# Kernel optimization log

Hardware: AMD Instinct MI355X
Metric: run time of the kernel (lower is better)

## Reference

```python
import jax, jax.numpy as jnp
import numpy as np

B, S, D_IN = 2, 2048, 2048
H, G, HD = 16, 4, 128          # num_heads, num_kv_groups, head_dim
GROUP = H // G                  # 4 query heads per kv group
D_OUT = H * HD                  # 2048
EPS = 1e-6


def _rope_tables(seq_len, head_dim, theta=10000.0):
    inv = 1.0 / (theta ** (np.arange(0, head_dim, 2, dtype=np.float32) / head_dim))
    pos = np.arange(seq_len, dtype=np.float32)
    ang = np.outer(pos, inv)                      # [S, HD/2]
    ang = np.concatenate([ang, ang], axis=-1)     # [S, HD]
    return jnp.asarray(np.cos(ang)), jnp.asarray(np.sin(ang))


def setup_inputs() -> dict:
    key = jax.random.key(0)
    ks = jax.random.split(key, 6)
    x = jax.random.normal(ks[0], (B, S, D_IN), dtype=jnp.float32)
    # Linear weights stored as [in, out] so y = x @ W (same math as nn.Linear)
    Wq = jax.random.normal(ks[1], (D_IN, 2 * D_OUT), dtype=jnp.float32) * (D_IN ** -0.5)
    Wk = jax.random.normal(ks[2], (D_IN, G * HD), dtype=jnp.float32) * (D_IN ** -0.5)
    Wv = jax.random.normal(ks[3], (D_IN, G * HD), dtype=jnp.float32) * (D_IN ** -0.5)
    Wo = jax.random.normal(ks[4], (D_OUT, D_IN), dtype=jnp.float32) * (D_OUT ** -0.5)
    q_norm_w = jnp.zeros((HD,), dtype=jnp.float32)  # Qwen-style zero-init (scale = 1 + w)
    k_norm_w = jnp.zeros((HD,), dtype=jnp.float32)
    cos, sin = _rope_tables(S, HD)
    mask = jnp.triu(jnp.ones((S, S), dtype=bool), k=1)  # causal: True above diagonal is masked
    return {"x": x, "Wq": Wq, "Wk": Wk, "Wv": Wv, "Wo": Wo,
            "q_norm_w": q_norm_w, "k_norm_w": k_norm_w,
            "cos": cos, "sin": sin, "mask": mask}


def _rmsnorm(x, w):
    xf = x.astype(jnp.float32)
    n = xf * jax.lax.rsqrt(jnp.mean(xf * xf, axis=-1, keepdims=True) + EPS)
    return (n * (1.0 + w.astype(jnp.float32))).astype(x.dtype)


def _apply_rope(x, cos, sin):
    # x: [..., S, HD]; full-dim rotation (rot_dim == head_dim)
    s = x.shape[-2]
    c = cos[:s][None, None]
    sn = sin[:s][None, None]
    x1, x2 = x[..., : HD // 2], x[..., HD // 2 :]
    rotated = jnp.concatenate([-x2, x1], axis=-1)
    return (x * c + rotated * sn).astype(x.dtype)


def reference(x, Wq, Wk, Wv, Wo, q_norm_w, k_norm_w, cos, sin, mask):
    b, s, _ = x.shape
    qg = (x @ Wq).reshape(b, s, H, 2 * HD)
    q, gate = qg[..., :HD], qg[..., HD:]
    gate = gate.reshape(b, s, D_OUT)
    q = q.transpose(0, 2, 1, 3)                                 # [b,H,s,HD]
    k = (x @ Wk).reshape(b, s, G, HD).transpose(0, 2, 1, 3)     # [b,G,s,HD]
    v = (x @ Wv).reshape(b, s, G, HD).transpose(0, 2, 1, 3)
    q = _rmsnorm(q, q_norm_w)
    k = _rmsnorm(k, k_norm_w)
    q = _apply_rope(q, cos, sin)
    k = _apply_rope(k, cos, sin)
    # GQA: group query heads by kv group instead of repeat_interleave on k/v
    qg4 = q.reshape(b, G, GROUP, s, HD)
    scores = jnp.einsum("bgjqd,bgkd->bgjqk", qg4, k)            # [b,G,GROUP,s,s]
    scores = jnp.where(mask[None, None, None], -jnp.inf, scores)
    w = jax.nn.softmax((scores * (HD ** -0.5)).astype(jnp.float32), axis=-1).astype(q.dtype)
    ctx = jnp.einsum("bgjqk,bgkd->bgjqd", w, v)                 # [b,G,GROUP,s,HD]
    ctx = ctx.reshape(b, H, s, HD).transpose(0, 2, 1, 3).reshape(b, s, D_OUT)
    ctx = ctx * jax.nn.sigmoid(gate)
    return ctx @ Wo
```

## Files before the change

### kernel.cpp

```cpp
#include <hip/hip_runtime.h>

#define S_LEN 2048
#define NROWS 4096
#define DIN   2048
#define DQKV  5120
#define DQG   4096

typedef __bf16 bf16x8 __attribute__((ext_vector_type(8)));
typedef float  floatx4 __attribute__((ext_vector_type(4)));
typedef unsigned short u16;

#define QK_SCALE 0.08838834764831845f

__device__ __forceinline__ u16 f2bf(float f) {
  unsigned int u = __float_as_uint(f);
  u += 0x7fffu + ((u >> 16) & 1u);
  return (u16)(u >> 16);
}
__device__ __forceinline__ float bf2f(u16 v) {
  return __uint_as_float(((unsigned int)v) << 16);
}
__device__ __forceinline__ int swz(int col, int row) {
  return (col & ~63) | ((((col >> 3) & 7) ^ (row & 7)) << 3) | (col & 7);
}

__device__ __forceinline__ void gload_lds16(const void* g, void* l) {
  __builtin_amdgcn_global_load_lds(
      (__attribute__((address_space(1))) void*)(void*)(g),
      (__attribute__((address_space(3))) void*)(l), 16, 0, 0);
}

__device__ __forceinline__ void tcvt_body(const float* __restrict__ src,
                                          u16* __restrict__ dst,
                                          int C, int dld, int bx, int by,
                                          float (*tile)[33]) {
  const int c0 = bx * 32, r0 = by * 32;
  const int t = threadIdx.x;
  {
    const int rl = t >> 3, cl4 = (t & 7) * 4;
    const float4 v = *reinterpret_cast<const float4*>(src + (size_t)(r0 + rl) * C + c0 + cl4);
    tile[rl][cl4 + 0] = v.x; tile[rl][cl4 + 1] = v.y;
    tile[rl][cl4 + 2] = v.z; tile[rl][cl4 + 3] = v.w;
  }
  __syncthreads();
  {
    const int cl = t >> 3, rl4 = (t & 7) * 4;
    ushort4 o;
    o.x = f2bf(tile[rl4 + 0][cl]); o.y = f2bf(tile[rl4 + 1][cl]);
    o.z = f2bf(tile[rl4 + 2][cl]); o.w = f2bf(tile[rl4 + 3][cl]);
    const int rd = c0 + cl, cd = r0 + rl4;
    *reinterpret_cast<ushort4*>(dst + (size_t)rd * dld + swz(cd, rd)) = o;
  }
}

__global__ __launch_bounds__(256) void prep(const float* __restrict__ x,
                                            const float* __restrict__ Wq,
                                            const float* __restrict__ Wk,
                                            const float* __restrict__ Wv,
                                            const float* __restrict__ Wo,
                                            u16* __restrict__ xb,
                                            u16* __restrict__ WqkvT,
                                            u16* __restrict__ WoT) {
  __shared__ float tile[32][33];
  const int bid = blockIdx.x;
  if (bid < 8192) {
    const int i = bid * 256 + threadIdx.x;
    const int row = i >> 9, col = (i & 511) << 2;
    const float4 v = reinterpret_cast<const float4*>(x)[i];
    ushort4 o;
    o.x = f2bf(v.x); o.y = f2bf(v.y); o.z = f2bf(v.z); o.w = f2bf(v.w);
    *reinterpret_cast<ushort4*>(xb + (size_t)row * DIN + swz(col, row)) = o;
  } else if (bid < 16384) {
    const int l = bid - 8192;
    tcvt_body(Wq, WqkvT, 4096, 2048, l & 127, l >> 7, tile);
  } else if (bid < 17408) {
    const int l = bid - 16384;
    tcvt_body(Wk, WqkvT + (size_t)4096 * 2048, 512, 2048, l & 15, l >> 4, tile);
  } else if (bid < 18432) {
    const int l = bid - 17408;
    tcvt_body(Wv, WqkvT + (size_t)4608 * 2048, 512, 2048, l & 15, l >> 4, tile);
  } else {
    const int l = bid - 18432;
    tcvt_body(Wo, WoT, 2048, 2048, l & 63, l >> 6, tile);
  }
}

template <bool BF16_OUT>
__global__ __launch_bounds__(256) void gemm_bt(const u16* __restrict__ A,
                                               const u16* __restrict__ Bt,
                                               void* __restrict__ Cv,
                                               int M, int N, int K, int ldc) {
  __shared__ __align__(16) u16 As[128 * 64];
  __shared__ __align__(16) u16 Bs[128 * 64];
  const int tid = threadIdx.x, wv = tid >> 6, lane = tid & 63;
  const int m0 = blockIdx.y * 128, n0 = blockIdx.x * 128;
  const int wm = (wv >> 1) * 64, wn = (wv & 1) * 64;
  const int frow = lane & 15, quad = lane >> 4, fsw = frow & 7;
  const int srow = lane >> 3, scol = (lane & 7) * 8;
  floatx4 acc[4][4] = {};
  for (int k0 = 0; k0 < K; k0 += 64) {
#pragma unroll
    for (int i = 0; i < 4; ++i) {
      const int rr = (wv * 4 + i) * 8;
      gload_lds16(A  + (size_t)(m0 + rr + srow) * K + k0 + scol, &As[rr * 64]);
      gload_lds16(Bt + (size_t)(n0 + rr + srow) * K + k0 + scol, &Bs[rr * 64]);
    }
    __syncthreads();
#pragma unroll
    for (int ks = 0; ks < 2; ++ks) {
      bf16x8 af[4], bfr[4];
#pragma unroll
      for (int mi = 0; mi < 4; ++mi)
        af[mi] = *reinterpret_cast<const bf16x8*>(
            &As[(wm + mi * 16 + frow) * 64 + (((ks * 4 + quad) ^ fsw) << 3)]);
#pragma unroll
      for (int ni = 0; ni < 4; ++ni)
        bfr[ni] = *reinterpret_cast<const bf16x8*>(
            &Bs[(wn + ni * 16 + frow) * 64 + (((ks * 4 + quad) ^ fsw) << 3)]);
#pragma unroll
      for (int mi = 0; mi < 4; ++mi)
#pragma unroll
        for (int ni = 0; ni < 4; ++ni)
          acc[mi][ni] = __builtin_amdgcn_mfma_f32_16x16x32_bf16(af[mi], bfr[ni], acc[mi][ni], 0, 0, 0);
    }
    __syncthreads();
  }
  const int crow = (lane >> 4) * 4, ccol = lane & 15;
#pragma unroll
  for (int mi = 0; mi < 4; ++mi)
#pragma unroll
    for (int ni = 0; ni < 4; ++ni) {
      const size_t base = (size_t)(m0 + wm + mi * 16 + crow) * ldc + (n0 + wn + ni * 16 + ccol);
      if constexpr (BF16_OUT) {
        u16* C = (u16*)Cv;
#pragma unroll
        for (int r = 0; r < 4; ++r) C[base + (size_t)r * ldc] = f2bf(acc[mi][ni][r]);
      } else {
        float* C = (float*)Cv;
#pragma unroll
        for (int r = 0; r < 4; ++r) C[base + (size_t)r * ldc] = acc[mi][ni][r];
      }
    }
}

__global__ __launch_bounds__(512, 2) void gemm256(const u16* __restrict__ A,
                                                  const u16* __restrict__ Bt,
                                                  u16* __restrict__ C,
                                                  int K, int ldc) {
  __shared__ __align__(16) u16 As[2][256 * 64];
  __shared__ __align__(16) u16 Bs[2][256 * 64];
  const int tid = threadIdx.x, wv = tid >> 6, lane = tid & 63;
  const int nx = gridDim.x;
  const int orig = blockIdx.y * nx + blockIdx.x;
  const int cpx = (nx * gridDim.y) >> 3;
  const int wgid = (orig & 7) * cpx + (orig >> 3);
  const int m0 = (wgid / nx) * 256, n0 = (wgid % nx) * 256;
  const int wm = (wv >> 2) * 128, wn = (wv & 3) * 64;
  const int f = lane & 15, quad = lane >> 4, fs = f & 7;

  const u16* Ab = A  + (size_t)(m0 + wv * 8 + (lane >> 3)) * K + (lane & 7) * 8;
  const u16* Bb = Bt + (size_t)(n0 + wv * 8 + (lane >> 3)) * K + (lane & 7) * 8;

  floatx4 acc[8][4] = {};
  bf16x8 af[4], bfr[4];

  auto stageA = [&](int sl, int t, int u) {
    gload_lds16(Ab + (size_t)u * 64 * K + (size_t)t * 64, &As[sl][(u * 64 + wv * 8) * 64]);
  };
  auto stageB = [&](int sl, int t, int u) {
    gload_lds16(Bb + (size_t)u * 64 * K + (size_t)t * 64, &Bs[sl][(u * 64 + wv * 8) * 64]);
  };
  auto loadA = [&](int sl, int fh, int ks) {
#pragma unroll
    for (int mf = 0; mf < 4; ++mf)
      af[mf] = *reinterpret_cast<const bf16x8*>(
          &As[sl][(wm + fh * 64 + mf * 16 + f) * 64 + ((((ks << 2) + quad) ^ fs) << 3)]);
  };
  auto loadB = [&](int sl, int ks) {
#pragma unroll
    for (int nf = 0; nf < 4; ++nf)
      bfr[nf] = *reinterpret_cast<const bf16x8*>(
          &Bs[sl][(wn + nf * 16 + f) * 64 + ((((ks << 2) + quad) ^ fs) << 3)]);
  };
  auto mmas = [&](int fh) {
#pragma unroll
    for (int mf = 0; mf < 4; ++mf)
#pragma unroll
      for (int nf = 0; nf < 4; ++nf)
        acc[fh * 4 + mf][nf] = __builtin_amdgcn_mfma_f32_16x16x32_bf16(
            af[mf], bfr[nf], acc[fh * 4 + mf][nf], 0, 0, 0);
  };

#pragma unroll
  for (int u = 0; u < 4; ++u) stageA(0, 0, u);
#pragma unroll
  for (int u = 0; u < 4; ++u) stageB(0, 0, u);
  stageA(1, 1, 0); stageA(1, 1, 2); stageB(1, 1, 0);
  asm volatile("s_waitcnt vmcnt(3)" ::: "memory");
  __builtin_amdgcn_s_barrier();

  const int IT = K >> 7;
#pragma unroll 1
  for (int i = 0; i < IT; ++i) {
    const int t0 = 2 * i;
    const bool st = (i < IT - 1);
    loadA(0, 0, 0); loadB(0, 0);
    stageA(1, t0 + 1, 1); stageA(1, t0 + 1, 3); stageB(1, t0 + 1, 1);
    __builtin_amdgcn_s_barrier();
    asm volatile("s_waitcnt lgkmcnt(0)" ::: "memory");
    __builtin_amdgcn_s_setprio(1); mmas(0); __builtin_amdgcn_s_setprio(0);
    __builtin_amdgcn_s_barrier();
    loadA(0, 1, 0);
    stageB(1, t0 + 1, 2); stageB(1, t0 + 1, 3);
    __builtin_amdgcn_s_barrier();
    asm volatile("s_waitcnt lgkmcnt(0)" ::: "memory");
    __builtin_amdgcn_s_setprio(1); mmas(1); __builtin_amdgcn_s_setprio(0);
    __builtin_amdgcn_s_barrier();
    loadA(0, 0, 1); loadB(0, 1);
    __builtin_amdgcn_s_barrier();
    asm volatile("s_waitcnt lgkmcnt(0)" ::: "memory");
    __builtin_amdgcn_s_setprio(1); mmas(0); __builtin_amdgcn_s_setprio(0);
    __builtin_amdgcn_s_barrier();
    loadA(0, 1, 1);
    if (st) { stageA(0, t0 + 2, 0); stageA(0, t0 + 2, 2); stageB(0, t0 + 2, 0); }
    __builtin_amdgcn_s_barrier();
    asm volatile("s_waitcnt lgkmcnt(0)" ::: "memory");
    __builtin_amdgcn_s_setprio(1); mmas(1); __builtin_amdgcn_s_setprio(0);
    if (st) { asm volatile("s_waitcnt vmcnt(3)" ::: "memory"); }
    else    { asm volatile("s_waitcnt vmcnt(0)" ::: "memory"); }
    __builtin_amdgcn_s_barrier();
    loadA(1, 0, 0); loadB(1, 0);
    if (st) { stageA(0, t0 + 2, 1); stageA(0, t0 + 2, 3); stageB(0, t0 + 2, 1); }
    __builtin_amdgcn_s_barrier();
    asm volatile("s_waitcnt lgkmcnt(0)" ::: "memory");
    __builtin_amdgcn_s_setprio(1); mmas(0); __builtin_amdgcn_s_setprio(0);
    __builtin_amdgcn_s_barrier();
    loadA(1, 1, 0);
    if (st) { stageB(0, t0 + 2, 2); stageB(0, t0 + 2, 3); }
    __builtin_amdgcn_s_barrier();
    asm volatile("s_waitcnt lgkmcnt(0)" ::: "memory");
    __builtin_amdgcn_s_setprio(1); mmas(1); __builtin_amdgcn_s_setprio(0);
    __builtin_amdgcn_s_barrier();
    loadA(1, 0, 1); loadB(1, 1);
    __builtin_amdgcn_s_barrier();
    asm volatile("s_waitcnt lgkmcnt(0)" ::: "memory");
    __builtin_amdgcn_s_setprio(1); mmas(0); __builtin_amdgcn_s_setprio(0);
    __builtin_amdgcn_s_barrier();
    loadA(1, 1, 1);
    if (st) { stageA(1, t0 + 3, 0); stageA(1, t0 + 3, 2); stageB(1, t0 + 3, 0); }
    __builtin_amdgcn_s_barrier();
    asm volatile("s_waitcnt lgkmcnt(0)" ::: "memory");
    __builtin_amdgcn_s_setprio(1); mmas(1); __builtin_amdgcn_s_setprio(0);
    if (st) { asm volatile("s_waitcnt vmcnt(3)" ::: "memory"); }
    __builtin_amdgcn_s_barrier();
  }

#pragma unroll
  for (int mf = 0; mf < 8; ++mf)
#pragma unroll
    for (int nf = 0; nf < 4; ++nf) {
      const size_t base = (size_t)(m0 + wm + (mf >> 2) * 64 + (mf & 3) * 16 + quad * 4) * ldc
                        + (n0 + wn + nf * 16 + f);
#pragma unroll
      for (int r = 0; r < 4; ++r) C[base + (size_t)r * ldc] = f2bf(acc[mf][nf][r]);
    }
}

__global__ __launch_bounds__(256) void postproj(const u16* __restrict__ QKV,
                                                const float* __restrict__ qw,
                                                const float* __restrict__ kw,
                                                const float* __restrict__ cosT,
                                                const float* __restrict__ sinT,
                                                u16* __restrict__ Qb,
                                                u16* __restrict__ Kb,
                                                u16* __restrict__ Vt) {
  __shared__ u16 tile[32][40];
  const int bid = blockIdx.x;
  const int wv = threadIdx.x >> 6, lane = threadIdx.x & 63;
  if (bid < 16384) {
    const int idx = bid * 4 + wv;
    const int h = idx & 15, row = idx >> 4;
    const int s = row & (S_LEN - 1), b = row >> 11;
    const u16* base = QKV + (size_t)row * DQKV + h * 256;
    const float v0 = bf2f(base[lane]), v1 = bf2f(base[lane + 64]);
    float ss = v0 * v0 + v1 * v1;
#pragma unroll
    for (int m = 32; m >= 1; m >>= 1) ss += __shfl_xor(ss, m);
    const float rn = rsqrtf(ss * (1.0f / 128.0f) + 1e-6f) * QK_SCALE;
    const float n0 = v0 * rn * (1.0f + qw[lane]);
    const float n1 = v1 * rn * (1.0f + qw[lane + 64]);
    const float c0 = cosT[(size_t)s * 128 + lane], c1 = cosT[(size_t)s * 128 + lane + 64];
    const float sn0 = sinT[(size_t)s * 128 + lane], sn1 = sinT[(size_t)s * 128 + lane + 64];
    u16* qb = Qb + ((size_t)(b * 16 + h) * S_LEN + s) * 128;
    qb[lane]      = f2bf(n0 * c0 - n1 * sn0);
    qb[lane + 64] = f2bf(n1 * c1 + n0 * sn1);
  } else if (bid < 20480) {
    const int idx = (bid - 16384) * 4 + wv;
    const int g = idx & 3, row = idx >> 2;
    const int s = row & (S_LEN - 1), b = row >> 11;
    const u16* base = QKV + (size_t)row * DQKV + DQG + g * 128;
    const float v0 = bf2f(base[lane]), v1 = bf2f(base[lane + 64]);
    float ss = v0 * v0 + v1 * v1;
#pragma unroll
    for (int m = 32; m >= 1; m >>= 1) ss += __shfl_xor(ss, m);
    const float rn = rsqrtf(ss * (1.0f / 128.0f) + 1e-6f);
    const float n0 = v0 * rn * (1.0f + kw[lane]);
    const float n1 = v1 * rn * (1.0f + kw[lane + 64]);
    const float c0 = cosT[(size_t)s * 128 + lane], c1 = cosT[(size_t)s * 128 + lane + 64];
    const float sn0 = sinT[(size_t)s * 128 + lane], sn1 = sinT[(size_t)s * 128 + lane + 64];
    u16* kb = Kb + ((size_t)(b * 4 + g) * S_LEN + s) * 128;
    const int sw = s & 7;
    const int d0 = lane, d1 = lane + 64;
    const int p0 = (((d0 >> 3) ^ sw) << 3) | (d0 & 7);
    const int p1 = (((d1 >> 3) ^ sw) << 3) | (d1 & 7);
    kb[p0] = f2bf(n0 * c0 - n1 * sn0);
    kb[p1] = f2bf(n1 * c1 + n0 * sn1);
  } else {
    const int l = bid - 20480;
    const int bg = l >> 8, rem = l & 255;
    const int d0 = ((rem >> 6) & 3) * 32, s0 = (rem & 63) * 32;
    const int b = bg >> 2, g = bg & 3;
    const int t = threadIdx.x;
    {
      const int sl = t >> 3, dl4 = (t & 7) * 4;
      const ushort4 v = *reinterpret_cast<const ushort4*>(
          QKV + (size_t)(b * S_LEN + s0 + sl) * DQKV + DQG + 512 + g * 128 + d0 + dl4);
      tile[sl][dl4 + 0] = v.x; tile[sl][dl4 + 1] = v.y;
      tile[sl][dl4 + 2] = v.z; tile[sl][dl4 + 3] = v.w;
    }
    __syncthreads();
    {
      const int dl = t >> 3, sl4 = (t & 7) * 4;
      ushort4 o;
      o.x = tile[sl4 + 0][dl]; o.y = tile[sl4 + 1][dl];
      o.z = tile[sl4 + 2][dl]; o.w = tile[sl4 + 3][dl];
      const int d = d0 + dl, s = s0 + sl4;
      const size_t base = (size_t)(bg * 128 + d) * S_LEN + (s & ~63);
      const int pos = ((((s >> 3) & 7) ^ (d & 7)) << 3) | (s & 7);
      *reinterpret_cast<ushort4*>(Vt + base + pos) = o;
    }
  }
}

__global__ __launch_bounds__(256) void attn(const u16* __restrict__ Qb,
                                            const u16* __restrict__ Kb,
                                            const u16* __restrict__ Vt,
                                            const u16* __restrict__ QKV,
                                            u16* __restrict__ ctxg) {
  __shared__ __align__(16) u16 Ks[2][64 * 128];
  __shared__ __align__(16) u16 Vts[2][128 * 64];
  __shared__ __align__(16) u16 Ps[4][16 * 64];
  const int tid = threadIdx.x, wv = tid >> 6, lane = tid & 63;
  const int ip = blockIdx.x, bh = blockIdx.y;
  const int b = bh >> 4, h = bh & 15, g = h >> 2, bg = b * 4 + g;
  const int f = lane & 15, quad = lane >> 4, fq = quad * 8;
  const int fsw = f & 7;
  const u16* Kp = Kb + (size_t)bg * S_LEN * 128;
  const u16* Vp = Vt + (size_t)bg * 128 * S_LEN;
  u16* Pw = Ps[wv];
  const int pwr_base = f * 64 + ((quad & 1) << 2);
  const int pf0_off = f * 64 + ((quad ^ fsw) << 3);
  const int pf1_off = f * 64 + (((4 + quad) ^ fsw) << 3);

  auto stage_k = [&](int sl, int kt) {
    const int k0 = kt * 64;
#pragma unroll
    for (int i = 0; i < 4; ++i) {
      const int j = wv * 4 + i;
      gload_lds16(Kp + (size_t)k0 * 128 + j * 512 + lane * 8, &Ks[sl][j * 512]);
    }
  };
  auto stage_v = [&](int sl, int kt) {
    const int k0 = kt * 64;
#pragma unroll
    for (int i = 0; i < 4; ++i) {
      const int r0 = (wv * 4 + i) * 8;
      gload_lds16(Vp + (size_t)(r0 + (lane >> 3)) * S_LEN + k0 + (lane & 7) * 8,
                  &Vts[sl][r0 * 64]);
    }
  };

  for (int pass = 0; pass < 2; ++pass) {
    const int qt = pass ? 31 - ip : ip;
    const int qrow = qt * 64 + wv * 16 + f;
    const u16* Qp = Qb + ((size_t)bh * S_LEN + qt * 64 + wv * 16) * 128;
    bf16x8 aq[4];
#pragma unroll
    for (int c = 0; c < 4; ++c)
      aq[c] = *reinterpret_cast<const bf16x8*>(&Qp[(size_t)f * 128 + c * 32 + fq]);

    floatx4 o[8] = {};
    float lsum = 0.f;
    const int nkt = qt + 1;

    __syncthreads();
    stage_k(0, 0); stage_v(0, 0);
    if (nkt > 1) {
      stage_k(1, 1); stage_v(1, 1);
      asm volatile("s_waitcnt vmcnt(8)" ::: "memory");
    } else {
      asm volatile("s_waitcnt vmcnt(0)" ::: "memory");
    }
    __syncthreads();

    {
      floatx4 sc[4] = {};
#pragma unroll
      for (int c = 0; c < 4; ++c)
#pragma unroll
        for (int n = 0; n < 4; ++n) {
          bf16x8 bk = *reinterpret_cast<const bf16x8*>(
              &Ks[0][(n * 16 + f) * 128 + (((4 * c + quad) ^ fsw) << 3)]);
          sc[n] = __builtin_amdgcn_mfma_f32_16x16x32_bf16(bk, aq[c], sc[n], 0, 0, 0);
        }
#pragma unroll
      for (int n = 0; n < 4; ++n) {
        float pv_[4];
#pragma unroll
        for (int r = 0; r < 4; ++r) {
          const int key = n * 16 + quad * 4 + r;
          const float p = (key <= qrow) ? __expf(sc[n][r]) : 0.f;
          lsum += p; pv_[r] = p;
        }
        ushort4 pk;
        pk.x = f2bf(pv_[0]); pk.y = f2bf(pv_[1]); pk.z = f2bf(pv_[2]); pk.w = f2bf(pv_[3]);
        *reinterpret_cast<ushort4*>(
            &Pw[pwr_base + (((2 * n + (quad >> 1)) ^ fsw) << 3)]) = pk;
      }
    }
    if (nkt > 1) {
      asm volatile("s_waitcnt vmcnt(4)" ::: "memory");
      __syncthreads();
    }

    int cur = 0;
    for (int t = 0; t < nkt; ++t) {
      const bool more = (t + 1 < nkt);
      floatx4 sn[4] = {};
      if (more) {
#pragma unroll
        for (int c = 0; c < 4; ++c)
#pragma unroll
          for (int n = 0; n < 4; ++n) {
            bf16x8 bk = *reinterpret_cast<const bf16x8*>(
                &Ks[cur ^ 1][(n * 16 + f) * 128 + (((4 * c + quad) ^ fsw) << 3)]);
            sn[n] = __builtin_amdgcn_mfma_f32_16x16x32_bf16(bk, aq[c], sn[n], 0, 0, 0);
          }
        if (t + 2 < nkt) stage_k(cur, t + 2);
      }
      bf16x8 pf0 = *reinterpret_cast<const bf16x8*>(&Pw[pf0_off]);
      bf16x8 pf1 = *reinterpret_cast<const bf16x8*>(&Pw[pf1_off]);
#pragma unroll
      for (int dt = 0; dt < 8; ++dt) {
        bf16x8 bv = *reinterpret_cast<const bf16x8*>(
            &Vts[cur][(dt * 16 + f) * 64 + ((quad ^ fsw) << 3)]);
        o[dt] = __builtin_amdgcn_mfma_f32_16x16x32_bf16(pf0, bv, o[dt], 0, 0, 0);
      }
#pragma unroll
      for (int dt = 0; dt < 8; ++dt) {
        bf16x8 bv = *reinterpret_cast<const bf16x8*>(
            &Vts[cur][(dt * 16 + f) * 64 + (((4 + quad) ^ fsw) << 3)]);
        o[dt] = __builtin_amdgcn_mfma_f32_16x16x32_bf16(pf1, bv, o[dt], 0, 0, 0);
      }
      if (more) {
        const int kb = (t + 1) * 64;
#pragma unroll
        for (int n = 0; n < 4; ++n) {
          float pv_[4];
#pragma unroll
          for (int r = 0; r < 4; ++r) {
            const int key = kb + n * 16 + quad * 4 + r;
            const float p = (key <= qrow) ? __expf(sn[n][r]) : 0.f;
            lsum += p; pv_[r] = p;
          }
          ushort4 pk;
          pk.x = f2bf(pv_[0]); pk.y = f2bf(pv_[1]); pk.z = f2bf(pv_[2]); pk.w = f2bf(pv_[3]);
          *reinterpret_cast<ushort4*>(
              &Pw[pwr_base + (((2 * n + (quad >> 1)) ^ fsw) << 3)]) = pk;
        }
        __syncthreads();
        if (t + 2 < nkt) {
          stage_v(cur, t + 2);
          asm volatile("s_waitcnt vmcnt(4)" ::: "memory");
        } else {
          asm volatile("s_waitcnt vmcnt(0)" ::: "memory");
        }
        __syncthreads();
        cur ^= 1;
      }
    }

    lsum += __shfl_xor(lsum, 16);
    lsum += __shfl_xor(lsum, 32);
    const float inv = 1.0f / lsum;

#pragma unroll
    for (int r = 0; r < 4; ++r) {
      const float linv = __shfl(inv, quad * 4 + r);
      const int s = qt * 64 + wv * 16 + quad * 4 + r;
      const size_t grow = (size_t)b * S_LEN + s;
#pragma unroll
      for (int dt = 0; dt < 8; ++dt) {
        const int d = dt * 16 + f;
        const float gate = bf2f(QKV[grow * DQKV + h * 256 + 128 + d]);
        const float val = o[dt][r] * linv * (1.0f / (1.0f + __expf(-gate)));
        const int col = h * 128 + d;
        ctxg[grow * 2048 + swz(col, (int)grow)] = f2bf(val);
      }
    }
  }
}

extern "C" void kernel_launch(void* const* d_in, const int* in_sizes, int n_in,
                              void* d_out, int out_size, void* d_ws, size_t ws_size,
                              hipStream_t stream) {
  const float* x    = (const float*)d_in[0];
  const float* Wq   = (const float*)d_in[1];
  const float* Wk   = (const float*)d_in[2];
  const float* Wv   = (const float*)d_in[3];
  const float* Wo   = (const float*)d_in[4];
  const float* qnw  = (const float*)d_in[5];
  const float* knw  = (const float*)d_in[6];
  const float* cosT = (const float*)d_in[7];
  const float* sinT = (const float*)d_in[8];

  char* p = (char*)d_ws;
  u16*   xb    = (u16*)p;  p += (size_t)NROWS * DIN * 2;
  u16*   WqkvT = (u16*)p;  p += (size_t)DQKV * DIN * 2;
  u16*   WoT   = (u16*)p;  p += (size_t)2048 * 2048 * 2;
  u16*   QKVb  = (u16*)p;  p += (size_t)NROWS * DQKV * 2;
  u16*   Qbf   = (u16*)p;  p += (size_t)2 * 16 * S_LEN * 128 * 2;
  u16*   Kbf   = (u16*)p;  p += (size_t)2 * 4 * S_LEN * 128 * 2;
  u16*   Vtb   = (u16*)p;  p += (size_t)2 * 4 * S_LEN * 128 * 2;
  u16*   ctxg  = (u16*)p;  p += (size_t)NROWS * 2048 * 2;

  prep<<<22528, 256, 0, stream>>>(x, Wq, Wk, Wv, Wo, xb, WqkvT, WoT);

  gemm256<<<dim3(16, 16), 512, 0, stream>>>(xb, WqkvT, QKVb, DIN, DQKV);
  gemm_bt<true><<<dim3(8, 32), 256, 0, stream>>>(
      xb, WqkvT + (size_t)4096 * 2048, QKVb + 4096, NROWS, 1024, DIN, DQKV);

  postproj<<<22528, 256, 0, stream>>>(QKVb, qnw, knw, cosT, sinT, Qbf, Kbf, Vtb);

  attn<<<dim3(16, 32), 256, 0, stream>>>(Qbf, Kbf, Vtb, QKVb, ctxg);

  gemm_bt<false><<<dim3(16, 32), 256, 0, stream>>>(ctxg, WoT, (float*)d_out, NROWS, 2048, 2048, 2048);
}
```

Before: 393.1 us.

## Process both paired query tiles in one pass sharing K/V tile loads

The attention kernel previously ran two sequential passes (query tile ip and 31-ip), each streaming its own K/V tiles. Now both query tiles are processed together in a single loop over key tiles, so each staged K/V tile feeds both tiles' MFMAs. The short tile is skipped once its causal range ends. The software pipeline is simplified to a single-stage prefetch with a full vmcnt(0) wait plus barrier per iteration. This roughly halves K/V global-to-LDS traffic and barrier count, at the cost of doubled accumulator registers (possible occupancy loss) and less overlap between loads and the QK/PV compute.

After: 491.9 us. +25.1%, slower.

```diff
diff --git a/kernel.cpp b/kernel.cpp
--- a/kernel.cpp
+++ b/kernel.cpp
@@ -349,7 +349,7 @@
                                             u16* __restrict__ ctxg) {
   __shared__ __align__(16) u16 Ks[2][64 * 128];
   __shared__ __align__(16) u16 Vts[2][128 * 64];
-  __shared__ __align__(16) u16 Ps[4][16 * 64];
+  __shared__ __align__(16) u16 Ps[4][2][16 * 64];
   const int tid = threadIdx.x, wv = tid >> 6, lane = tid & 63;
   const int ip = blockIdx.x, bh = blockIdx.y;
   const int b = bh >> 4, h = bh & 15, g = h >> 2, bg = b * 4 + g;
@@ -357,7 +357,8 @@
   const int fsw = f & 7;
   const u16* Kp = Kb + (size_t)bg * S_LEN * 128;
   const u16* Vp = Vt + (size_t)bg * 128 * S_LEN;
-  u16* Pw = Ps[wv];
+  u16* PwA = Ps[wv][0];
+  u16* PwB = Ps[wv][1];
   const int pwr_base = f * 64 + ((quad & 1) << 2);
   const int pf0_off = f * 64 + ((quad ^ fsw) << 3);
   const int pf1_off = f * 64 + (((4 + quad) ^ fsw) << 3);
@@ -380,133 +381,129 @@
     }
   };
 
-  for (int pass = 0; pass < 2; ++pass) {
-    const int qt = pass ? 31 - ip : ip;
-    const int qrow = qt * 64 + wv * 16 + f;
-    const u16* Qp = Qb + ((size_t)bh * S_LEN + qt * 64 + wv * 16) * 128;
-    bf16x8 aq[4];
-#pragma unroll
-    for (int c = 0; c < 4; ++c)
-      aq[c] = *reinterpret_cast<const bf16x8*>(&Qp[(size_t)f * 128 + c * 32 + fq]);
-
-    floatx4 o[8] = {};
-    float lsum = 0.f;
-    const int nkt = qt + 1;
-
-    __syncthreads();
-    stage_k(0, 0); stage_v(0, 0);
-    if (nkt > 1) {
-      stage_k(1, 1); stage_v(1, 1);
-      asm volatile("s_waitcnt vmcnt(8)" ::: "memory");
-    } else {
-      asm volatile("s_waitcnt vmcnt(0)" ::: "memory");
-    }
-    __syncthreads();
+  const int qtA = ip, qtB = 31 - ip;
+  const int nkt = qtB + 1;
+  const int qrowA = qtA * 64 + wv * 16 + f;
+  const int qrowB = qtB * 64 + wv * 16 + f;
+  const u16* QpA = Qb + ((size_t)bh * S_LEN + qtA * 64 + wv * 16) * 128;
+  const u16* QpB = Qb + ((size_t)bh * S_LEN + qtB * 64 + wv * 16) * 128;
+  bf16x8 aqA[4], aqB[4];
+#pragma unroll
+  for (int c = 0; c < 4; ++c) {
+    aqA[c] = *reinterpret_cast<const bf16x8*>(&QpA[(size_t)f * 128 + c * 32 + fq]);
+    aqB[c] = *reinterpret_cast<const bf16x8*>(&QpB[(size_t)f * 128 + c * 32 + fq]);
+  }
+
+  floatx4 oA[8] = {}, oB[8] = {};
+  float lsA = 0.f, lsB = 0.f;
+
+  stage_k(0, 0); stage_v(0, 0);
+  asm volatile("s_waitcnt vmcnt(0)" ::: "memory");
+  __syncthreads();
+
+  int cur = 0;
+  for (int t = 0; t < nkt; ++t) {
+    const bool doA = (t <= qtA);
+    if (t + 1 < nkt) { stage_k(cur ^ 1, t + 1); stage_v(cur ^ 1, t + 1); }
+    const int kb = t * 64;
 
     {
-      floatx4 sc[4] = {};
+      floatx4 scB[4] = {}, scA[4] = {};
 #pragma unroll
       for (int c = 0; c < 4; ++c)
 #pragma unroll
         for (int n = 0; n < 4; ++n) {
           bf16x8 bk = *reinterpret_cast<const bf16x8*>(
-              &Ks[0][(n * 16 + f) * 128 + (((4 * c + quad) ^ fsw) << 3)]);
-          sc[n] = __builtin_amdgcn_mfma_f32_16x16x32_bf16(bk, aq[c], sc[n], 0, 0, 0);
+              &Ks[cur][(n * 16 + f) * 128 + (((4 * c + quad) ^ fsw) << 3)]);
+          scB[n] = __builtin_amdgcn_mfma_f32_16x16x32_bf16(bk, aqB[c], scB[n], 0, 0, 0);
+          if (doA)
+            scA[n] = __builtin_amdgcn_mfma_f32_16x16x32_bf16(bk, aqA[c], scA[n], 0, 0, 0);
         }
 #pragma unroll
       for (int n = 0; n < 4; ++n) {
         float pv_[4];
 #pragma unroll
         for (int r = 0; r < 4; ++r) {
-          const int key = n * 16 + quad * 4 + r;
-          const float p = (key <= qrow) ? __expf(sc[n][r]) : 0.f;
-          lsum += p; pv_[r] = p;
+          const int key = kb + n * 16 + quad * 4 + r;
+          const float p = (key <= qrowB) ? __expf(scB[n][r]) : 0.f;
+          lsB += p; pv_[r] = p;
         }
         ushort4 pk;
         pk.x = f2bf(pv_[0]); pk.y = f2bf(pv_[1]); pk.z = f2bf(pv_[2]); pk.w = f2bf(pv_[3]);
         *reinterpret_cast<ushort4*>(
-            &Pw[pwr_base + (((2 * n + (quad >> 1)) ^ fsw) << 3)]) = pk;
+            &PwB[pwr_base + (((2 * n + (quad >> 1)) ^ fsw) << 3)]) = pk;
       }
-    }
-    if (nkt > 1) {
-      asm volatile("s_waitcnt vmcnt(4)" ::: "memory");
-      __syncthreads();
-    }
-
-    int cur = 0;
-    for (int t = 0; t < nkt; ++t) {
-      const bool more = (t + 1 < nkt);
-      floatx4 sn[4] = {};
-      if (more) {
-#pragma unroll
-        for (int c = 0; c < 4; ++c)
-#pragma unroll
-          for (int n = 0; n < 4; ++n) {
-            bf16x8 bk = *reinterpret_cast<const bf16x8*>(
-                &Ks[cur ^ 1][(n * 16 + f) * 128 + (((4 * c + quad) ^ fsw) << 3)]);
-            sn[n] = __builtin_amdgcn_mfma_f32_16x16x32_bf16(bk, aq[c], sn[n], 0, 0, 0);
-          }
-        if (t + 2 < nkt) stage_k(cur, t + 2);
-      }
-      bf16x8 pf0 = *reinterpret_cast<const bf16x8*>(&Pw[pf0_off]);
-      bf16x8 pf1 = *reinterpret_cast<const bf16x8*>(&Pw[pf1_off]);
-#pragma unroll
-      for (int dt = 0; dt < 8; ++dt) {
-        bf16x8 bv = *reinterpret_cast<const bf16x8*>(
-            &Vts[cur][(dt * 16 + f) * 64 + ((quad ^ fsw) << 3)]);
-        o[dt] = __builtin_amdgcn_mfma_f32_16x16x32_bf16(pf0, bv, o[dt], 0, 0, 0);
-      }
-#pragma unroll
-      for (int dt = 0; dt < 8; ++dt) {
-        bf16x8 bv = *reinterpret_cast<const bf16x8*>(
-            &Vts[cur][(dt * 16 + f) * 64 + (((4 + quad) ^ fsw) << 3)]);
-        o[dt] = __builtin_amdgcn_mfma_f32_16x16x32_bf16(pf1, bv, o[dt], 0, 0, 0);
-      }
-      if (more) {
-        const int kb = (t + 1) * 64;
+      if (doA) {
 #pragma unroll
         for (int n = 0; n < 4; ++n) {
           float pv_[4];
 #pragma unroll
           for (int r = 0; r < 4; ++r) {
             const int key = kb + n * 16 + quad * 4 + r;
-            const float p = (key <= qrow) ? __expf(sn[n][r]) : 0.f;
-            lsum += p; pv_[r] = p;
+            const float p = (key <= qrowA) ? __expf(scA[n][r]) : 0.f;
+            lsA += p; pv_[r] = p;
           }
           ushort4 pk;
           pk.x = f2bf(pv_[0]); pk.y = f2bf(pv_[1]); pk.z = f2bf(pv_[2]); pk.w = f2bf(pv_[3]);
           *reinterpret_cast<ushort4*>(
-              &Pw[pwr_base + (((2 * n + (quad >> 1)) ^ fsw) << 3)]) = pk;
+              &PwA[pwr_base + (((2 * n + (quad >> 1)) ^ fsw) << 3)]) = pk;
         }
-        __syncthreads();
-        if (t + 2 < nkt) {
-          stage_v(cur, t + 2);
-          asm volatile("s_waitcnt vmcnt(4)" ::: "memory");
-        } else {
-          asm volatile("s_waitcnt vmcnt(0)" ::: "memory");
-        }
-        __syncthreads();
-        cur ^= 1;
       }
     }
 
-    lsum += __shfl_xor(lsum, 16);
-    lsum += __shfl_xor(lsum, 32);
-    const float inv = 1.0f / lsum;
-
-#pragma unroll
-    for (int r = 0; r < 4; ++r) {
-      const float linv = __shfl(inv, quad * 4 + r);
-      const int s = qt * 64 + wv * 16 + quad * 4 + r;
-      const size_t grow = (size_t)b * S_LEN + s;
+    {
+      bf16x8 pB0 = *reinterpret_cast<const bf16x8*>(&PwB[pf0_off]);
+      bf16x8 pB1 = *reinterpret_cast<const bf16x8*>(&PwB[pf1_off]);
+      bf16x8 pA0, pA1;
+      if (doA) {
+        pA0 = *reinterpret_cast<const bf16x8*>(&PwA[pf0_off]);
+        pA1 = *reinterpret_cast<const bf16x8*>(&PwA[pf1_off]);
+      }
 #pragma unroll
       for (int dt = 0; dt < 8; ++dt) {
-        const int d = dt * 16 + f;
-        const float gate = bf2f(QKV[grow * DQKV + h * 256 + 128 + d]);
-        const float val = o[dt][r] * linv * (1.0f / (1.0f + __expf(-gate)));
-        const int col = h * 128 + d;
-        ctxg[grow * 2048 + swz(col, (int)grow)] = f2bf(val);
+        bf16x8 bv = *reinterpret_cast<const bf16x8*>(
+            &Vts[cur][(dt * 16 + f) * 64 + ((quad ^ fsw) << 3)]);
+        oB[dt] = __builtin_amdgcn_mfma_f32_16x16x32_bf16(pB0, bv, oB[dt], 0, 0, 0);
+        if (doA)
+          oA[dt] = __builtin_amdgcn_mfma_f32_16x16x32_bf16(pA0, bv, oA[dt], 0, 0, 0);
       }
+#pragma unroll
+      for (int dt = 0; dt < 8; ++dt) {
+        bf16x8 bv = *reinterpret_cast<const bf16x8*>(
+            &Vts[cur][(dt * 16 + f) * 64 + (((4 + quad) ^ fsw) << 3)]);
+        oB[dt] = __builtin_amdgcn_mfma_f32_16x16x32_bf16(pB1, bv, oB[dt], 0, 0, 0);
+        if (doA)
+          oA[dt] = __builtin_amdgcn_mfma_f32_16x16x32_bf16(pA1, bv, oA[dt], 0, 0, 0);
+      }
+    }
+
+    asm volatile("s_waitcnt vmcnt(0)" ::: "memory");
+    __syncthreads();
+    cur ^= 1;
+  }
+
+  lsA += __shfl_xor(lsA, 16); lsA += __shfl_xor(lsA, 32);
+  lsB += __shfl_xor(lsB, 16); lsB += __shfl_xor(lsB, 32);
+  const float invA = 1.0f / lsA, invB = 1.0f / lsB;
+
+#pragma unroll
+  for (int r = 0; r < 4; ++r) {
+    const float linvA = __shfl(invA, quad * 4 + r);
+    const float linvB = __shfl(invB, quad * 4 + r);
+    const int sA = qtA * 64 + wv * 16 + quad * 4 + r;
+    const int sB = qtB * 64 + wv * 16 + quad * 4 + r;
+    const size_t growA = (size_t)b * S_LEN + sA;
+    const size_t growB = (size_t)b * S_LEN + sB;
+#pragma unroll
+    for (int dt = 0; dt < 8; ++dt) {
+      const int d = dt * 16 + f;
+      const int col = h * 128 + d;
+      const float gateA = bf2f(QKV[growA * DQKV + h * 256 + 128 + d]);
+      const float valA = oA[dt][r] * linvA * (1.0f / (1.0f + __expf(-gateA)));
+      ctxg[growA * 2048 + swz(col, (int)growA)] = f2bf(valA);
+      const float gateB = bf2f(QKV[growB * DQKV + h * 256 + 128 + d]);
+      const float valB = oB[dt][r] * linvB * (1.0f / (1.0f + __expf(-gateB)));
+      ctxg[growB * 2048 + swz(col, (int)growB)] = f2bf(valB);
     }
   }
 }
```

## Replace double-buffered paired-tile attention with single-buffer one-tile-per-block scheduling

Applied to the files above, without the earlier changes.

The attention kernel previously had each block process two query tiles (ip and 31-ip) and double-buffer K/V in LDS, so QK^T of the next tile overlapped PV of the current one. It now launches twice as many blocks, one query tile each, in a longest-first interleaved order. K/V sit in a single LDS buffer and each iteration does load, wait, compute, sync in sequence. This halves LDS per block, which may allow more resident blocks and better load balance across CUs, but it drops the software pipelining, so global-load latency is exposed every iteration.

Measured after the change: 416.1 us. +5.9%, slower.

```diff
diff --git a/kernel.cpp b/kernel.cpp
--- a/kernel.cpp
+++ b/kernel.cpp
@@ -347,11 +347,12 @@
                                             const u16* __restrict__ Vt,
                                             const u16* __restrict__ QKV,
                                             u16* __restrict__ ctxg) {
-  __shared__ __align__(16) u16 Ks[2][64 * 128];
-  __shared__ __align__(16) u16 Vts[2][128 * 64];
+  __shared__ __align__(16) u16 Ks[64 * 128];
+  __shared__ __align__(16) u16 Vts[128 * 64];
   __shared__ __align__(16) u16 Ps[4][16 * 64];
   const int tid = threadIdx.x, wv = tid >> 6, lane = tid & 63;
   const int ip = blockIdx.x, bh = blockIdx.y;
+  const int qt = (ip & 1) ? (ip >> 1) : 31 - (ip >> 1);
   const int b = bh >> 4, h = bh & 15, g = h >> 2, bg = b * 4 + g;
   const int f = lane & 15, quad = lane >> 4, fq = quad * 8;
   const int fsw = f & 7;
@@ -362,151 +363,94 @@
   const int pf0_off = f * 64 + ((quad ^ fsw) << 3);
   const int pf1_off = f * 64 + (((4 + quad) ^ fsw) << 3);
 
-  auto stage_k = [&](int sl, int kt) {
-    const int k0 = kt * 64;
-#pragma unroll
-    for (int i = 0; i < 4; ++i) {
-      const int j = wv * 4 + i;
-      gload_lds16(Kp + (size_t)k0 * 128 + j * 512 + lane * 8, &Ks[sl][j * 512]);
-    }
-  };
-  auto stage_v = [&](int sl, int kt) {
-    const int k0 = kt * 64;
-#pragma unroll
-    for (int i = 0; i < 4; ++i) {
-      const int r0 = (wv * 4 + i) * 8;
-      gload_lds16(Vp + (size_t)(r0 + (lane >> 3)) * S_LEN + k0 + (lane & 7) * 8,
-                  &Vts[sl][r0 * 64]);
-    }
-  };
-
-  for (int pass = 0; pass < 2; ++pass) {
-    const int qt = pass ? 31 - ip : ip;
-    const int qrow = qt * 64 + wv * 16 + f;
-    const u16* Qp = Qb + ((size_t)bh * S_LEN + qt * 64 + wv * 16) * 128;
-    bf16x8 aq[4];
+  const int nkt = qt + 1;
+  const int qrow = qt * 64 + wv * 16 + f;
+  const u16* Qp = Qb + ((size_t)bh * S_LEN + qt * 64 + wv * 16) * 128;
+  bf16x8 aq[4];
+#pragma unroll
+  for (int c = 0; c < 4; ++c)
+    aq[c] = *reinterpret_cast<const bf16x8*>(&Qp[(size_t)f * 128 + c * 32 + fq]);
+
+  floatx4 o[8] = {};
+  float lsum = 0.f;
+
+  for (int t = 0; t < nkt; ++t) {
+    const int kb = t * 64;
+    {
+      const int k0 = kb;
+#pragma unroll
+      for (int i = 0; i < 4; ++i) {
+        const int j = wv * 4 + i;
+        gload_lds16(Kp + (size_t)k0 * 128 + j * 512 + lane * 8, &Ks[j * 512]);
+      }
+#pragma unroll
+      for (int i = 0; i < 4; ++i) {
+        const int r0 = (wv * 4 + i) * 8;
+        gload_lds16(Vp + (size_t)(r0 + (lane >> 3)) * S_LEN + k0 + (lane & 7) * 8,
+                    &Vts[r0 * 64]);
+      }
+    }
+    asm volatile("s_waitcnt vmcnt(0)" ::: "memory");
+    __syncthreads();
+
+    floatx4 sc[4] = {};
 #pragma unroll
     for (int c = 0; c < 4; ++c)
-      aq[c] = *reinterpret_cast<const bf16x8*>(&Qp[(size_t)f * 128 + c * 32 + fq]);
-
-    floatx4 o[8] = {};
-    float lsum = 0.f;
-    const int nkt = qt + 1;
-
+#pragma unroll
+      for (int n = 0; n < 4; ++n) {
+        bf16x8 bk = *reinterpret_cast<const bf16x8*>(
+            &Ks[(n * 16 + f) * 128 + (((4 * c + quad) ^ fsw) << 3)]);
+        sc[n] = __builtin_amdgcn_mfma_f32_16x16x32_bf16(bk, aq[c], sc[n], 0, 0, 0);
+      }
+
+#pragma unroll
+    for (int n = 0; n < 4; ++n) {
+      float pv_[4];
+#pragma unroll
+      for (int r = 0; r < 4; ++r) {
+        const int key = kb + n * 16 + quad * 4 + r;
+        const float p = (key <= qrow) ? __expf(sc[n][r]) : 0.f;
+        lsum += p; pv_[r] = p;
+      }
+      ushort4 pk;
+      pk.x = f2bf(pv_[0]); pk.y = f2bf(pv_[1]); pk.z = f2bf(pv_[2]); pk.w = f2bf(pv_[3]);
+      *reinterpret_cast<ushort4*>(
+          &Pw[pwr_base + (((2 * n + (quad >> 1)) ^ fsw) << 3)]) = pk;
+    }
+
+    bf16x8 pf0 = *reinterpret_cast<const bf16x8*>(&Pw[pf0_off]);
+    bf16x8 pf1 = *reinterpret_cast<const bf16x8*>(&Pw[pf1_off]);
+#pragma unroll
+    for (int dt = 0; dt < 8; ++dt) {
+      bf16x8 bv = *reinterpret_cast<const bf16x8*>(
+          &Vts[(dt * 16 + f) * 64 + ((quad ^ fsw) << 3)]);
+      o[dt] = __builtin_amdgcn_mfma_f32_16x16x32_bf16(pf0, bv, o[dt], 0, 0, 0);
+    }
+#pragma unroll
+    for (int dt = 0; dt < 8; ++dt) {
+      bf16x8 bv = *reinterpret_cast<const bf16x8*>(
+          &Vts[(dt * 16 + f) * 64 + (((4 + quad) ^ fsw) << 3)]);
+      o[dt] = __builtin_amdgcn_mfma_f32_16x16x32_bf16(pf1, bv, o[dt], 0, 0, 0);
+    }
     __syncthreads();
-    stage_k(0, 0); stage_v(0, 0);
-    if (nkt > 1) {
-      stage_k(1, 1); stage_v(1, 1);
-      asm volatile("s_waitcnt vmcnt(8)" ::: "memory");
-    } else {
-      asm volatile("s_waitcnt vmcnt(0)" ::: "memory");
-    }
-    __syncthreads();
-
-    {
-      floatx4 sc[4] = {};
-#pragma unroll
-      for (int c = 0; c < 4; ++c)
-#pragma unroll
-        for (int n = 0; n < 4; ++n) {
-          bf16x8 bk = *reinterpret_cast<const bf16x8*>(
-              &Ks[0][(n * 16 + f) * 128 + (((4 * c + quad) ^ fsw) << 3)]);
-          sc[n] = __builtin_amdgcn_mfma_f32_16x16x32_bf16(bk, aq[c], sc[n], 0, 0, 0);
-        }
-#pragma unroll
-      for (int n = 0; n < 4; ++n) {
-        float pv_[4];
-#pragma unroll
-        for (int r = 0; r < 4; ++r) {
-          const int key = n * 16 + quad * 4 + r;
-          const float p = (key <= qrow) ? __expf(sc[n][r]) : 0.f;
-          lsum += p; pv_[r] = p;
-        }
-        ushort4 pk;
-        pk.x = f2bf(pv_[0]); pk.y = f2bf(pv_[1]); pk.z = f2bf(pv_[2]); pk.w = f2bf(pv_[3]);
-        *reinterpret_cast<ushort4*>(
-            &Pw[pwr_base + (((2 * n + (quad >> 1)) ^ fsw) << 3)]) = pk;
-      }
-    }
-    if (nkt > 1) {
-      asm volatile("s_waitcnt vmcnt(4)" ::: "memory");
-      __syncthreads();
-    }
-
-    int cur = 0;
-    for (int t = 0; t < nkt; ++t) {
-      const bool more = (t + 1 < nkt);
-      floatx4 sn[4] = {};
-      if (more) {
-#pragma unroll
-        for (int c = 0; c < 4; ++c)
-#pragma unroll
-          for (int n = 0; n < 4; ++n) {
-            bf16x8 bk = *reinterpret_cast<const bf16x8*>(
-                &Ks[cur ^ 1][(n * 16 + f) * 128 + (((4 * c + quad) ^ fsw) << 3)]);
-            sn[n] = __builtin_amdgcn_mfma_f32_16x16x32_bf16(bk, aq[c], sn[n], 0, 0, 0);
-          }
-        if (t + 2 < nkt) stage_k(cur, t + 2);
-      }
-      bf16x8 pf0 = *reinterpret_cast<const bf16x8*>(&Pw[pf0_off]);
-      bf16x8 pf1 = *reinterpret_cast<const bf16x8*>(&Pw[pf1_off]);
-#pragma unroll
-      for (int dt = 0; dt < 8; ++dt) {
-        bf16x8 bv = *reinterpret_cast<const bf16x8*>(
-            &Vts[cur][(dt * 16 + f) * 64 + ((quad ^ fsw) << 3)]);
-        o[dt] = __builtin_amdgcn_mfma_f32_16x16x32_bf16(pf0, bv, o[dt], 0, 0, 0);
-      }
-#pragma unroll
-      for (int dt = 0; dt < 8; ++dt) {
-        bf16x8 bv = *reinterpret_cast<const bf16x8*>(
-            &Vts[cur][(dt * 16 + f) * 64 + (((4 + quad) ^ fsw) << 3)]);
-        o[dt] = __builtin_amdgcn_mfma_f32_16x16x32_bf16(pf1, bv, o[dt], 0, 0, 0);
-      }
-      if (more) {
-        const int kb = (t + 1) * 64;
-#pragma unroll
-        for (int n = 0; n < 4; ++n) {
-          float pv_[4];
-#pragma unroll
-          for (int r = 0; r < 4; ++r) {
-            const int key = kb + n * 16 + quad * 4 + r;
-            const float p = (key <= qrow) ? __expf(sn[n][r]) : 0.f;
-            lsum += p; pv_[r] = p;
-          }
-          ushort4 pk;
-          pk.x = f2bf(pv_[0]); pk.y = f2bf(pv_[1]); pk.z = f2bf(pv_[2]); pk.w = f2bf(pv_[3]);
-          *reinterpret_cast<ushort4*>(
-              &Pw[pwr_base + (((2 * n + (quad >> 1)) ^ fsw) << 3)]) = pk;
-        }
-        __syncthreads();
-        if (t + 2 < nkt) {
-          stage_v(cur, t + 2);
-          asm volatile("s_waitcnt vmcnt(4)" ::: "memory");
-        } else {
-          asm volatile("s_waitcnt vmcnt(0)" ::: "memory");
-        }
-        __syncthreads();
-        cur ^= 1;
-      }
-    }
-
-    lsum += __shfl_xor(lsum, 16);
-    lsum += __shfl_xor(lsum, 32);
-    const float inv = 1.0f / lsum;
-
-#pragma unroll
-    for (int r = 0; r < 4; ++r) {
-      const float linv = __shfl(inv, quad * 4 + r);
-      const int s = qt * 64 + wv * 16 + quad * 4 + r;
-      const size_t grow = (size_t)b * S_LEN + s;
-#pragma unroll
-      for (int dt = 0; dt < 8; ++dt) {
-        const int d = dt * 16 + f;
-        const float gate = bf2f(QKV[grow * DQKV + h * 256 + 128 + d]);
-        const float val = o[dt][r] * linv * (1.0f / (1.0f + __expf(-gate)));
-        const int col = h * 128 + d;
-        ctxg[grow * 2048 + swz(col, (int)grow)] = f2bf(val);
-      }
+  }
+
+  lsum += __shfl_xor(lsum, 16);
+  lsum += __shfl_xor(lsum, 32);
+  const float inv = 1.0f / lsum;
+
+#pragma unroll
+  for (int r = 0; r < 4; ++r) {
+    const float linv = __shfl(inv, quad * 4 + r);
+    const int s = qt * 64 + wv * 16 + quad * 4 + r;
+    const size_t grow = (size_t)b * S_LEN + s;
+#pragma unroll
+    for (int dt = 0; dt < 8; ++dt) {
+      const int d = dt * 16 + f;
+      const float gate = bf2f(QKV[grow * DQKV + h * 256 + 128 + d]);
+      const float val = o[dt][r] * linv * (1.0f / (1.0f + __expf(-gate)));
+      const int col = h * 128 + d;
+      ctxg[grow * 2048 + swz(col, (int)grow)] = f2bf(val);
     }
   }
 }
@@ -542,7 +486,7 @@
 
   postproj<<<22528, 256, 0, stream>>>(QKVb, qnw, knw, cosT, sinT, Qbf, Kbf, Vtb);
 
-  attn<<<dim3(16, 32), 256, 0, stream>>>(Qbf, Kbf, Vtb, QKVb, ctxg);
+  attn<<<dim3(32, 32), 256, 0, stream>>>(Qbf, Kbf, Vtb, QKVb, ctxg);
 
   gemm_bt<false><<<dim3(16, 32), 256, 0, stream>>>(ctxg, WoT, (float*)d_out, NROWS, 2048, 2048, 2048);
 }
```
